# Kernel tuning notes

Measured on AMD Instinct MI355X. Metric: run time of the kernel, lower is better.

Reference implementation:

```python
import jax, jax.numpy as jnp
import numpy as np

B, T, C = 2, 2048, 1024
E = 8            # num_experts
K = 2            # num_active (top-k)
H = 4 * C        # expert hidden dim


def setup_inputs() -> dict:
    key = jax.random.key(0)
    ks = jax.random.split(key, 8)
    s = 0.02
    return {
        "x": jax.random.normal(ks[0], (B, T, C), dtype=jnp.float32),
        "Wg": jax.random.normal(ks[1], (C, E), dtype=jnp.float32) * s,
        "bg": jnp.zeros((E,), dtype=jnp.float32),
        "W1": jax.random.normal(ks[2], (E, C, H), dtype=jnp.float32) * s,
        "b1": jnp.zeros((E, H), dtype=jnp.float32),
        "W2": jax.random.normal(ks[3], (E, H, C), dtype=jnp.float32) * s,
        "b2": jnp.zeros((E, C), dtype=jnp.float32),
    }


def reference(x, Wg, bg, W1, b1, W2, b2):
    Bs, Ts, Cs = x.shape
    x_flat = x.reshape(-1, Cs)                       # [N, C]
    gate_logits = x_flat @ Wg + bg                   # [N, E]
    gates = jax.nn.softmax(gate_logits, axis=-1)
    w, idx = jax.lax.top_k(gates, K)                 # [N, K]
    w = w / jnp.sum(w, axis=-1, keepdims=True)
    # combine[n, e] = sum_k w[n,k] * (idx[n,k] == e); zero for unrouted experts,
    # so weighting the dense per-expert output reproduces the masked scatter-add.
    combine = jnp.sum(jax.nn.one_hot(idx, E, dtype=x.dtype) * w[..., None], axis=1)  # [N, E]
    out = jnp.zeros_like(x_flat)
    for e in range(E):  # small fixed expert loop; GEMM-dominated
        h = jax.nn.gelu(x_flat @ W1[e] + b1[e], approximate=False)  # [N, H]
        y = h @ W2[e] + b2[e]                                       # [N, C]
        out = out + y * combine[:, e:e + 1]
    return out.reshape(Bs, Ts, Cs)
```

## Files before the change

kernel.cpp:

```cpp
#include <hip/hip_runtime.h>
#include <hip/hip_bf16.h>
#include <math.h>

#define NTOK  4096
#define CDIM  1024
#define HDIM  4096
#define NEXP  8
#define TOPK  2

using short8 = __attribute__((ext_vector_type(8))) short;
using f32x4  = __attribute__((ext_vector_type(4))) float;
using us4    = __attribute__((ext_vector_type(4))) unsigned short;

__device__ inline ushort f2bf(float f) {
    uint32_t u = __builtin_bit_cast(uint32_t, f);
    uint32_t r = (u + 0x7FFFu + ((u >> 16) & 1u)) >> 16;
    return (ushort)r;
}

__device__ __forceinline__ void gl_lds16(const void* g, void* l) {
    __builtin_amdgcn_global_load_lds(
        (const __attribute__((address_space(1))) void*)(void*)g,
        (__attribute__((address_space(3))) void*)l, 16, 0, 0);
}

__global__ __launch_bounds__(256)
void gate_kernel(const float* __restrict__ x, const float* __restrict__ Wg,
                 const float* __restrict__ bg, int* __restrict__ counts,
                 int* __restrict__ tlist, float* __restrict__ wslot,
                 ushort* __restrict__ xbf) {
    int wave = threadIdx.x >> 6, lane = threadIdx.x & 63;
    int t = blockIdx.x * 4 + wave;
    const float* xr = x + (size_t)t * CDIM;

    float acc[NEXP];
#pragma unroll
    for (int e = 0; e < NEXP; e++) acc[e] = 0.f;

#pragma unroll
    for (int i = 0; i < CDIM / 64; i++) {
        int c = lane + 64 * i;
        float xv = xr[c];
        xbf[(size_t)t * CDIM + c] = f2bf(xv);
        const float* wr = Wg + (size_t)c * NEXP;
#pragma unroll
        for (int e = 0; e < NEXP; e++) acc[e] += xv * wr[e];
    }
#pragma unroll
    for (int e = 0; e < NEXP; e++) {
        float v = acc[e];
        for (int off = 32; off > 0; off >>= 1) v += __shfl_xor(v, off);
        acc[e] = v + bg[e];
    }
    if (lane == 0) {
        int i1 = 0; float m1 = acc[0];
#pragma unroll
        for (int e = 1; e < NEXP; e++) if (acc[e] > m1) { m1 = acc[e]; i1 = e; }
        int i2 = -1; float m2 = -1e30f;
#pragma unroll
        for (int e = 0; e < NEXP; e++) if (e != i1 && acc[e] > m2) { m2 = acc[e]; i2 = e; }
        float w0 = 1.f / (1.f + expf(m2 - m1));
        float w1 = 1.f - w0;
        int p0 = atomicAdd(&counts[i1], 1);
        tlist[i1 * NTOK + p0] = t * 2;
        int p1 = atomicAdd(&counts[i2], 1);
        tlist[i2 * NTOK + p1] = t * 2 + 1;
        wslot[t * 2]     = w0;
        wslot[t * 2 + 1] = w1;
    }
}

__global__ __launch_bounds__(256)
void transpose_kernel(const float* __restrict__ in, ushort* __restrict__ out,
                      int R, int Ccols) {
    __shared__ float tile[64][65];
    int e = blockIdx.z;
    const float* src = in + (size_t)e * R * Ccols;
    ushort* dst = out + (size_t)e * Ccols * R;
    int c0 = blockIdx.x * 64, r0 = blockIdx.y * 64;
    int tid = threadIdx.x;
    int tx = tid & 15, ty = tid >> 4;
#pragma unroll
    for (int j = 0; j < 4; j++) {
        int r = ty + 16 * j;
        float4 v = *(const float4*)&src[(size_t)(r0 + r) * Ccols + c0 + tx * 4];
        tile[r][tx * 4 + 0] = v.x;
        tile[r][tx * 4 + 1] = v.y;
        tile[r][tx * 4 + 2] = v.z;
        tile[r][tx * 4 + 3] = v.w;
    }
    __syncthreads();
#pragma unroll
    for (int j = 0; j < 4; j++) {
        int c = ty + 16 * j;
        us4 o;
#pragma unroll
        for (int i = 0; i < 4; i++) o[i] = f2bf(tile[tx * 4 + i][c]);
        *(us4*)&dst[(size_t)(c0 + c) * R + r0 + tx * 4] = o;
    }
}

template<int GELU, int OUTBF16>
__global__ __launch_bounds__(256, 3)
void moe_gemm(const ushort* __restrict__ A, const ushort* __restrict__ Bt,
              const float* __restrict__ bias, const int* __restrict__ tlist,
              const int* __restrict__ counts, void* __restrict__ Out,
              int K, int N, int ashift, int nxmask, int nxshift, int ksplit,
              size_t psz) {
    int e = blockIdx.z;
    int cnt = counts[e];
    int m0 = blockIdx.y * 128;
    if (m0 >= cnt) return;
    int n0 = (blockIdx.x & nxmask) * 128;
    int split = blockIdx.x >> nxshift;
    int kbeg = split * ksplit;

    __shared__ ushort As[2][128 * 32];
    __shared__ ushort Bs[2][128 * 32];
    __shared__ int rowv[128];

    int tid = threadIdx.x;
    if (tid < 128) {
        int r = m0 + tid;
        rowv[tid] = tlist[e * NTOK + (r < cnt ? r : cnt - 1)];
    }
    __syncthreads();

    const ushort* Be = Bt + (size_t)e * N * K;

    int lane = tid & 63, w = tid >> 6;
    int wm = (w >> 1) * 64, wn = (w & 1) * 64;
    int quad = lane >> 4, l16 = lane & 15;

    int srow   = tid >> 2;
    int schunk = (tid & 3) ^ ((tid >> 3) & 3);
    const ushort* pa0 = A  + (size_t)(rowv[srow]      >> ashift) * K + kbeg + schunk * 8;
    const ushort* pa1 = A  + (size_t)(rowv[srow + 64] >> ashift) * K + kbeg + schunk * 8;
    const ushort* pb0 = Be + (size_t)(n0 + srow)      * K + kbeg + schunk * 8;
    const ushort* pb1 = Be + (size_t)(n0 + srow + 64) * K + kbeg + schunk * 8;

    int swr  = quad ^ ((l16 >> 1) & 3);
    int aidx = (wm + l16) * 32 + swr * 8;
    int bidx = (wn + l16) * 32 + swr * 8;

    f32x4 acc[4][4] = {};

    auto STAGE = [&](int buf) {
        gl_lds16(pa0, &As[buf][(w * 16) * 32]);
        gl_lds16(pa1, &As[buf][(w * 16 + 64) * 32]);
        gl_lds16(pb0, &Bs[buf][(w * 16) * 32]);
        gl_lds16(pb1, &Bs[buf][(w * 16 + 64) * 32]);
        pa0 += 32; pa1 += 32; pb0 += 32; pb1 += 32;
    };
    auto COMPUTE = [&](int buf) {
        short8 a[4], b[4];
#pragma unroll
        for (int mt = 0; mt < 4; mt++) a[mt] = *(short8*)&As[buf][aidx + mt * 512];
#pragma unroll
        for (int nt = 0; nt < 4; nt++) b[nt] = *(short8*)&Bs[buf][bidx + nt * 512];
#pragma unroll
        for (int mt = 0; mt < 4; mt++)
#pragma unroll
            for (int nt = 0; nt < 4; nt++)
                acc[mt][nt] = __builtin_amdgcn_mfma_f32_16x16x32_bf16(
                    a[mt], b[nt], acc[mt][nt], 0, 0, 0);
    };

    int nsteps = ksplit >> 5;
    STAGE(0);
    __syncthreads();
    for (int i = 0; i < nsteps - 2; i += 2) {
        STAGE(1);
        COMPUTE(0);
        __syncthreads();
        STAGE(0);
        COMPUTE(1);
        __syncthreads();
    }
    STAGE(1);
    COMPUTE(0);
    __syncthreads();
    COMPUTE(1);

    float* outF = (float*)Out + split * psz;
    ushort* outH = (ushort*)Out;
    const float* be = bias + (size_t)e * N;
#pragma unroll
    for (int mt = 0; mt < 4; mt++) {
#pragma unroll
        for (int r = 0; r < 4; r++) {
            int lrow = wm + mt * 16 + quad * 4 + r;
            if (m0 + lrow < cnt) {
                int v = rowv[lrow];
                size_t base = (size_t)v * N;
#pragma unroll
                for (int nt = 0; nt < 4; nt++) {
                    int col = n0 + wn + nt * 16 + l16;
                    float val = acc[mt][nt][r] + (split == 0 ? be[col] : 0.f);
                    if (GELU) val = 0.5f * val * (1.0f + erff(val * 0.70710678118654752f));
                    if (OUTBF16) outH[base + col] = f2bf(val);
                    else         outF[base + col] = val;
                }
            }
        }
    }
}

__global__ __launch_bounds__(256)
void combine_kernel(const float* __restrict__ y, const float* __restrict__ wslot,
                    float* __restrict__ out) {
    const float* y2 = y + (size_t)NTOK * TOPK * CDIM;
    int idx = blockIdx.x * 256 + threadIdx.x;
    int c4 = idx & (CDIM / 4 - 1);
    int t = idx >> 8;
    float w0 = wslot[2 * t], w1 = wslot[2 * t + 1];
    const float4* y0a = (const float4*)(y  + (size_t)(2 * t) * CDIM);
    const float4* y1a = (const float4*)(y  + (size_t)(2 * t + 1) * CDIM);
    const float4* y0b = (const float4*)(y2 + (size_t)(2 * t) * CDIM);
    const float4* y1b = (const float4*)(y2 + (size_t)(2 * t + 1) * CDIM);
    float4 a0 = y0a[c4], a1 = y0b[c4], b0 = y1a[c4], b1 = y1b[c4], o;
    o.x = w0 * (a0.x + a1.x) + w1 * (b0.x + b1.x);
    o.y = w0 * (a0.y + a1.y) + w1 * (b0.y + b1.y);
    o.z = w0 * (a0.z + a1.z) + w1 * (b0.z + b1.z);
    o.w = w0 * (a0.w + a1.w) + w1 * (b0.w + b1.w);
    ((float4*)(out + (size_t)t * CDIM))[c4] = o;
}

extern "C" void kernel_launch(void* const* d_in, const int* in_sizes, int n_in,
                              void* d_out, int out_size, void* d_ws, size_t ws_size,
                              hipStream_t stream) {
    const float* x  = (const float*)d_in[0];
    const float* Wg = (const float*)d_in[1];
    const float* bg = (const float*)d_in[2];
    const float* W1 = (const float*)d_in[3];
    const float* b1 = (const float*)d_in[4];
    const float* W2 = (const float*)d_in[5];
    const float* b2 = (const float*)d_in[6];
    float* out = (float*)d_out;
    char* ws = (char*)d_ws;

    size_t off = 0;
    int*    counts = (int*)(ws + off);    off += 256;
    int*    tlist  = (int*)(ws + off);    off += (size_t)NEXP * NTOK * 4;
    float*  wslot  = (float*)(ws + off);  off += (size_t)NTOK * TOPK * 4;
    ushort* xbf    = (ushort*)(ws + off); off += (size_t)NTOK * CDIM * 2;
    ushort* WT     = (ushort*)(ws + off); off += (size_t)NEXP * CDIM * HDIM * 2;
    ushort* h      = (ushort*)(ws + off); off += (size_t)NTOK * TOPK * HDIM * 2;
    float*  y      = (float*)(ws + off);  off += (size_t)NTOK * TOPK * CDIM * 4 * 2;

    hipMemsetAsync(counts, 0, NEXP * sizeof(int), stream);

    gate_kernel<<<NTOK / 4, 256, 0, stream>>>(x, Wg, bg, counts, tlist, wslot, xbf);

    transpose_kernel<<<dim3(HDIM / 64, CDIM / 64, NEXP), 256, 0, stream>>>(
        W1, WT, CDIM, HDIM);

    moe_gemm<1, 1><<<dim3(HDIM / 128, NTOK / 128, NEXP), 256, 0, stream>>>(
        xbf, WT, b1, tlist, counts, (void*)h, CDIM, HDIM, 1,
        HDIM / 128 - 1, 5, CDIM, 0);

    transpose_kernel<<<dim3(CDIM / 64, HDIM / 64, NEXP), 256, 0, stream>>>(
        W2, WT, HDIM, CDIM);

    moe_gemm<0, 0><<<dim3((CDIM / 128) * 2, NTOK / 128, NEXP), 256, 0, stream>>>(
        h, WT, b2, tlist, counts, (void*)y, HDIM, CDIM, 0,
        CDIM / 128 - 1, 3, HDIM / 2, (size_t)NTOK * TOPK * CDIM);

    combine_kernel<<<(NTOK * CDIM / 4) / 256, 256, 0, stream>>>(y, wslot, out);
}
```

Measured before the change: 702.7 us.

## Rework weight transpose with bf16 swizzled LDS and interleave experts in GEMM grid

The weight transpose now converts to bf16 before writing to shared memory. It uses a 128-byte-row XOR-swizzled tile so that each thread reads and writes 16-byte vectors, which cuts LDS traffic and makes the global stores wider. The MoE GEMMs switch from a 3D grid to a flat 1D grid with the expert index in the low bits. Consecutive blocks therefore cover different experts, spreading the skipped (empty) tiles and the load evenly across CUs. The swizzle indexing is more intricate and has to exactly match the read pattern.

```diff
diff --git a/kernel.cpp b/kernel.cpp
--- a/kernel.cpp
+++ b/kernel.cpp
@@ -10,7 +10,6 @@
 
 using short8 = __attribute__((ext_vector_type(8))) short;
 using f32x4  = __attribute__((ext_vector_type(4))) float;
-using us4    = __attribute__((ext_vector_type(4))) unsigned short;
 
 __device__ inline ushort f2bf(float f) {
     uint32_t u = __builtin_bit_cast(uint32_t, f);
@@ -73,30 +72,38 @@
 __global__ __launch_bounds__(256)
 void transpose_kernel(const float* __restrict__ in, ushort* __restrict__ out,
                       int R, int Ccols) {
-    __shared__ float tile[64][65];
+    __shared__ ushort tile[64 * 64];
     int e = blockIdx.z;
     const float* src = in + (size_t)e * R * Ccols;
     ushort* dst = out + (size_t)e * Ccols * R;
     int c0 = blockIdx.x * 64, r0 = blockIdx.y * 64;
     int tid = threadIdx.x;
     int tx = tid & 15, ty = tid >> 4;
-#pragma unroll
-    for (int j = 0; j < 4; j++) {
-        int r = ty + 16 * j;
-        float4 v = *(const float4*)&src[(size_t)(r0 + r) * Ccols + c0 + tx * 4];
-        tile[r][tx * 4 + 0] = v.x;
-        tile[r][tx * 4 + 1] = v.y;
-        tile[r][tx * 4 + 2] = v.z;
-        tile[r][tx * 4 + 3] = v.w;
-    }
-    __syncthreads();
-#pragma unroll
-    for (int j = 0; j < 4; j++) {
-        int c = ty + 16 * j;
-        us4 o;
-#pragma unroll
-        for (int i = 0; i < 4; i++) o[i] = f2bf(tile[tx * 4 + i][c]);
-        *(us4*)&dst[(size_t)(c0 + c) * R + r0 + tx * 4] = o;
+
+    float4 v[4];
+#pragma unroll
+    for (int j = 0; j < 4; j++)
+        v[j] = *(const float4*)&src[(size_t)(r0 + ty * 4 + j) * Ccols + c0 + tx * 4];
+
+#pragma unroll
+    for (int i = 0; i < 4; i++) {
+        int c = tx * 4 + i;
+        uint2 pr;
+        pr.x = (uint)f2bf(v[0][i]) | ((uint)f2bf(v[1][i]) << 16);
+        pr.y = (uint)f2bf(v[2][i]) | ((uint)f2bf(v[3][i]) << 16);
+        int gr = (ty >> 1) ^ ((c >> 2) & 7);
+        int off = c * 128 + (gr << 4) + (ty & 1) * 8;
+        *(uint2*)((char*)tile + off) = pr;
+    }
+    __syncthreads();
+
+#pragma unroll
+    for (int p = 0; p < 2; p++) {
+        int c   = (tid >> 3) + 32 * p;
+        int rch = tid & 7;
+        int gr  = rch ^ ((c >> 2) & 7);
+        short8 val = *(short8*)((char*)tile + c * 128 + (gr << 4));
+        *(short8*)&dst[(size_t)(c0 + c) * R + r0 + rch * 8] = val;
     }
 }
 
@@ -107,12 +114,16 @@
               const int* __restrict__ counts, void* __restrict__ Out,
               int K, int N, int ashift, int nxmask, int nxshift, int ksplit,
               size_t psz) {
-    int e = blockIdx.z;
+    int flat = blockIdx.x;
+    int e  = flat & 7;
+    int j  = flat >> 3;
+    int mt = j & 31;
+    int nj = j >> 5;
     int cnt = counts[e];
-    int m0 = blockIdx.y * 128;
+    int m0 = mt * 128;
     if (m0 >= cnt) return;
-    int n0 = (blockIdx.x & nxmask) * 128;
-    int split = blockIdx.x >> nxshift;
+    int n0 = (nj & nxmask) * 128;
+    int split = nj >> nxshift;
     int kbeg = split * ksplit;
 
     __shared__ ushort As[2][128 * 32];
@@ -155,15 +166,15 @@
     auto COMPUTE = [&](int buf) {
         short8 a[4], b[4];
 #pragma unroll
-        for (int mt = 0; mt < 4; mt++) a[mt] = *(short8*)&As[buf][aidx + mt * 512];
-#pragma unroll
-        for (int nt = 0; nt < 4; nt++) b[nt] = *(short8*)&Bs[buf][bidx + nt * 512];
-#pragma unroll
-        for (int mt = 0; mt < 4; mt++)
-#pragma unroll
-            for (int nt = 0; nt < 4; nt++)
-                acc[mt][nt] = __builtin_amdgcn_mfma_f32_16x16x32_bf16(
-                    a[mt], b[nt], acc[mt][nt], 0, 0, 0);
+        for (int mti = 0; mti < 4; mti++) a[mti] = *(short8*)&As[buf][aidx + mti * 512];
+#pragma unroll
+        for (int nti = 0; nti < 4; nti++) b[nti] = *(short8*)&Bs[buf][bidx + nti * 512];
+#pragma unroll
+        for (int mti = 0; mti < 4; mti++)
+#pragma unroll
+            for (int nti = 0; nti < 4; nti++)
+                acc[mti][nti] = __builtin_amdgcn_mfma_f32_16x16x32_bf16(
+                    a[mti], b[nti], acc[mti][nti], 0, 0, 0);
     };
 
     int nsteps = ksplit >> 5;
@@ -186,17 +197,17 @@
     ushort* outH = (ushort*)Out;
     const float* be = bias + (size_t)e * N;
 #pragma unroll
-    for (int mt = 0; mt < 4; mt++) {
+    for (int mti = 0; mti < 4; mti++) {
 #pragma unroll
         for (int r = 0; r < 4; r++) {
-            int lrow = wm + mt * 16 + quad * 4 + r;
+            int lrow = wm + mti * 16 + quad * 4 + r;
             if (m0 + lrow < cnt) {
                 int v = rowv[lrow];
                 size_t base = (size_t)v * N;
 #pragma unroll
-                for (int nt = 0; nt < 4; nt++) {
-                    int col = n0 + wn + nt * 16 + l16;
-                    float val = acc[mt][nt][r] + (split == 0 ? be[col] : 0.f);
+                for (int nti = 0; nti < 4; nti++) {
+                    int col = n0 + wn + nti * 16 + l16;
+                    float val = acc[mti][nti][r] + (split == 0 ? be[col] : 0.f);
                     if (GELU) val = 0.5f * val * (1.0f + erff(val * 0.70710678118654752f));
                     if (OUTBF16) outH[base + col] = f2bf(val);
                     else         outF[base + col] = val;
@@ -255,14 +266,14 @@
     transpose_kernel<<<dim3(HDIM / 64, CDIM / 64, NEXP), 256, 0, stream>>>(
         W1, WT, CDIM, HDIM);
 
-    moe_gemm<1, 1><<<dim3(HDIM / 128, NTOK / 128, NEXP), 256, 0, stream>>>(
+    moe_gemm<1, 1><<<NEXP * 32 * (HDIM / 128), 256, 0, stream>>>(
         xbf, WT, b1, tlist, counts, (void*)h, CDIM, HDIM, 1,
         HDIM / 128 - 1, 5, CDIM, 0);
 
     transpose_kernel<<<dim3(CDIM / 64, HDIM / 64, NEXP), 256, 0, stream>>>(
         W2, WT, HDIM, CDIM);
 
-    moe_gemm<0, 0><<<dim3((CDIM / 128) * 2, NTOK / 128, NEXP), 256, 0, stream>>>(
+    moe_gemm<0, 0><<<NEXP * 32 * (CDIM / 128) * 2, 256, 0, stream>>>(
         h, WT, b2, tlist, counts, (void*)y, HDIM, CDIM, 0,
         CDIM / 128 - 1, 3, HDIM / 2, (size_t)NTOK * TOPK * CDIM);
 
```

After: 687.4 us. 1.02x faster.
